# Performance work log

Hardware: AMD Instinct MI355X
Metric: run time of the kernel (lower is better)

The kernel has to match this reference:

```python
import jax, jax.numpy as jnp
import numpy as np

N, E, B = 40000, 640000, 256
F_IN, H, D = 128, 128, 128  # num_node_features, hidden_dim, last_dim
EPS = 1e-5


def sage_conv(x, src, dst, Wl, bl, Wr, num_nodes):
    # PyG SAGEConv (mean aggr): out = lin_l(mean_j x_j) + lin_r(x)
    msg = x[src]                                            # [E, d] gather
    agg = jax.ops.segment_sum(msg, dst, num_segments=num_nodes)
    cnt = jax.ops.segment_sum(jnp.ones((src.shape[0],), x.dtype), dst,
                              num_segments=num_nodes)
    mean = agg / jnp.maximum(cnt, 1.0)[:, None]
    return mean @ Wl.T + bl + x @ Wr.T


def bn_eval(x, g, b, rm, rv):
    return g * (x - rm) * jax.lax.rsqrt(rv + EPS) + b


def lstm_cell(inp, h, c, Wih, Whh, bih, bhh):
    gates = inp @ Wih.T + h @ Whh.T + bih + bhh             # [B, 4D]
    i, f, g, o = jnp.split(gates, 4, axis=-1)
    c = jax.nn.sigmoid(f) * c + jax.nn.sigmoid(i) * jnp.tanh(g)
    h = jax.nn.sigmoid(o) * jnp.tanh(c)
    return h, c


def set2set(x, batch, Wih, Whh, bih, bhh, num_graphs, steps=3):
    d = x.shape[1]
    q_star = jnp.zeros((num_graphs, 2 * d), x.dtype)
    h = jnp.zeros((num_graphs, d), x.dtype)
    c = jnp.zeros((num_graphs, d), x.dtype)
    for _ in range(steps):
        h, c = lstm_cell(q_star, h, c, Wih, Whh, bih, bhh)
        q = h                                               # [B, D]
        e = jnp.sum(x * q[batch], axis=-1)                  # [N]
        emax = jax.ops.segment_max(e, batch, num_segments=num_graphs)
        a = jnp.exp(e - emax[batch])
        denom = jax.ops.segment_sum(a, batch, num_segments=num_graphs)
        a = a / denom[batch]
        r = jax.ops.segment_sum(a[:, None] * x, batch, num_segments=num_graphs)
        q_star = jnp.concatenate([q, r], axis=-1)
    return q_star


def setup_inputs() -> dict:
    key = jax.random.key(0)
    ks = jax.random.split(key, 20)
    x = jax.random.normal(ks[0], (N, F_IN), jnp.float32)
    edge_index = jax.random.randint(ks[1], (2, E), 0, N)
    batch = jnp.sort(jax.random.randint(ks[2], (N,), 0, B))
    s1, s2, sd = 1.0 / np.sqrt(F_IN), 1.0 / np.sqrt(H), 1.0 / np.sqrt(D)
    return {
        "x": x, "edge_index": edge_index, "batch": batch,
        "W1l": jax.random.normal(ks[3], (H, F_IN)) * s1,
        "b1l": jnp.zeros((H,)),
        "W1r": jax.random.normal(ks[4], (H, F_IN)) * s1,
        "g1": jnp.ones((H,)), "beta1": jnp.zeros((H,)),
        "rm1": jax.random.normal(ks[5], (H,)) * 0.1,
        "rv1": jax.random.uniform(ks[6], (H,), minval=0.5, maxval=1.5),
        "W2l": jax.random.normal(ks[7], (D, H)) * s2,
        "b2l": jnp.zeros((D,)),
        "W2r": jax.random.normal(ks[8], (D, H)) * s2,
        "g2": jnp.ones((D,)), "beta2": jnp.zeros((D,)),
        "rm2": jax.random.normal(ks[9], (D,)) * 0.1,
        "rv2": jax.random.uniform(ks[10], (D,), minval=0.5, maxval=1.5),
        "Wih": jax.random.normal(ks[11], (4 * D, 2 * D)) * sd,
        "Whh": jax.random.normal(ks[12], (4 * D, D)) * sd,
        "bih": jnp.zeros((4 * D,)), "bhh": jnp.zeros((4 * D,)),
        "Wp": jax.random.normal(ks[13], (D, 2 * D)) * sd,
        "bp": jnp.zeros((D,)),
    }


def reference(x, edge_index, batch, W1l, b1l, W1r, g1, beta1, rm1, rv1,
              W2l, b2l, W2r, g2, beta2, rm2, rv2, Wih, Whh, bih, bhh, Wp, bp):
    src, dst = edge_index[0], edge_index[1]
    num_nodes = x.shape[0]
    h1 = jax.nn.relu(bn_eval(sage_conv(x, src, dst, W1l, b1l, W1r, num_nodes),
                             g1, beta1, rm1, rv1))
    # dropout is identity in eval mode
    h2 = jax.nn.relu(bn_eval(sage_conv(h1, src, dst, W2l, b2l, W2r, num_nodes),
                             g2, beta2, rm2, rv2))
    q_star = set2set(h2, batch, Wih, Whh, bih, bhh, B, steps=3)  # [B, 2D]
    return q_star @ Wp.T + bp                                    # [B, D]
```

## Files before the change

kernel.cpp:

```cpp
#include <hip/hip_runtime.h>
#include <hip/hip_bf16.h>
#include <math.h>

#define NN 40000
#define NE 640000
#define NG 256
#define FD 128
#define SLOT 96
#define CSTR 32

typedef __attribute__((ext_vector_type(8))) short bf16x8;
typedef __attribute__((ext_vector_type(4))) float f32x4;

__device__ __forceinline__ float sigf(float x) { return 1.f / (1.f + __expf(-x)); }
__device__ __forceinline__ unsigned short f2b(float f) {
    unsigned int u = __float_as_uint(f);
    return (unsigned short)((u + 0x7FFFu + ((u >> 16) & 1u)) >> 16);
}
__device__ __forceinline__ float b2f(unsigned int u16) {
    return __uint_as_float(u16 << 16);
}

__global__ __launch_bounds__(256) void k_fused1(
    const float* __restrict__ A,
    const float* __restrict__ W1l, const float* __restrict__ W1r,
    unsigned short* __restrict__ C,
    const int* __restrict__ ei, const int* __restrict__ batch,
    int* __restrict__ gptr, int* __restrict__ dcnt, int* __restrict__ srcs,
    const float* __restrict__ W2l, const float* __restrict__ W2r,
    unsigned short* __restrict__ Wb,
    const float* __restrict__ Wihf, const float* __restrict__ Whhf,
    unsigned short* __restrict__ Wb2)
{
    __shared__ unsigned short Ws[128 * 128];
    int bid = blockIdx.x, t = threadIdx.x;

    if ((bid < 2012) && (bid & 1)) {
        int sidx = bid >> 1;
        if (sidx < 625) {
            int i = sidx * 256 + t;
            int4 s4 = ((const int4*)ei)[i];
            int4 d4 = ((const int4*)(ei + NE))[i];
            int p0 = atomicAdd(&dcnt[d4.x * CSTR], 1);
            if (p0 < SLOT) srcs[d4.x * SLOT + p0] = s4.x;
            int p1 = atomicAdd(&dcnt[d4.y * CSTR], 1);
            if (p1 < SLOT) srcs[d4.y * SLOT + p1] = s4.y;
            int p2 = atomicAdd(&dcnt[d4.z * CSTR], 1);
            if (p2 < SLOT) srcs[d4.z * SLOT + p2] = s4.z;
            int p3 = atomicAdd(&dcnt[d4.w * CSTR], 1);
            if (p3 < SLOT) srcs[d4.w * SLOT + p3] = s4.w;
        } else if (sidx < 782) {
            int i = (sidx - 625) * 256 + t;
            if (i >= NN) return;
            int b = batch[i];
            int pb = (i == 0) ? -1 : batch[i - 1];
            for (int g = pb + 1; g <= b; g++) gptr[g] = i;
            if (i == NN - 1)
                for (int g = b + 1; g <= NG; g++) gptr[g] = NN;
        } else if (sidx < 814) {
            int j4 = (sidx - 782) * 256 + t;
            int seg = j4 >> 12, off4 = j4 & 4095;
            const float* W = seg ? W2r : W2l;
            float4 v = ((const float4*)W)[off4];
            ushort4 o;
            o.x = f2b(v.x); o.y = f2b(v.y); o.z = f2b(v.z); o.w = f2b(v.w);
            *(ushort4*)(Wb + (size_t)j4 * 4) = o;
        } else {
            int j4 = (sidx - 814) * 256 + t;
            float4 v;
            size_t off;
            if (j4 < 32768) {
                int r = j4 >> 6, f4 = j4 & 63;
                int c = f4 >> 1, h = f4 & 1;
                v = ((const float4*)Wihf)[j4];
                off = ((size_t)c * 512 + r) * 8 + h * 4;
            } else {
                int jj = j4 - 32768;
                int r = jj >> 5, f4 = jj & 31;
                int c = f4 >> 1, h = f4 & 1;
                v = ((const float4*)Whhf)[jj];
                off = (size_t)512 * 256 + ((size_t)c * 512 + r) * 8 + h * 4;
            }
            ushort4 o;
            o.x = f2b(v.x); o.y = f2b(v.y); o.z = f2b(v.z); o.w = f2b(v.w);
            *(ushort4*)(Wb2 + off) = o;
        }
        return;
    }

    int mblk2 = (bid < 2012) ? (bid >> 1) : (bid - 1006);
    int nh = mblk2 & 1;
    int mblk = mblk2 >> 1;
    {
        const float* Wsrc = nh ? W1r : W1l;
#pragma unroll
        for (int i = 0; i < 8; i++) {
            int f = i * 256 + t;
            int row = f >> 4, c = f & 15;
            float4 u0 = *(const float4*)(Wsrc + row * 128 + c * 8);
            float4 u1 = *(const float4*)(Wsrc + row * 128 + c * 8 + 4);
            unsigned short tmp[8];
            tmp[0] = f2b(u0.x); tmp[1] = f2b(u0.y); tmp[2] = f2b(u0.z); tmp[3] = f2b(u0.w);
            tmp[4] = f2b(u1.x); tmp[5] = f2b(u1.y); tmp[6] = f2b(u1.z); tmp[7] = f2b(u1.w);
            int cs = c ^ (row & 15);
            *(uint4*)&Ws[row * 128 + cs * 8] = *(const uint4*)tmp;
        }
    }
    __syncthreads();
    int w = t >> 6, lane = t & 63;
    int ln = lane & 15, quad = lane >> 4;
    int m0 = mblk * 64 + w * 16;
    bf16x8 a[4];
    {
        const float* Arow = A + (size_t)(m0 + ln) * 128;
#pragma unroll
        for (int ks = 0; ks < 4; ks++) {
            float4 u0 = *(const float4*)(Arow + ks * 32 + quad * 8);
            float4 u1 = *(const float4*)(Arow + ks * 32 + quad * 8 + 4);
            unsigned short tmp[8];
            tmp[0] = f2b(u0.x); tmp[1] = f2b(u0.y); tmp[2] = f2b(u0.z); tmp[3] = f2b(u0.w);
            tmp[4] = f2b(u1.x); tmp[5] = f2b(u1.y); tmp[6] = f2b(u1.z); tmp[7] = f2b(u1.w);
            a[ks] = *(const bf16x8*)tmp;
        }
    }
    for (int nt = 0; nt < 8; nt++) {
        int n0 = nt * 16;
        int row = n0 + ln;
        f32x4 acc = {0.f, 0.f, 0.f, 0.f};
#pragma unroll
        for (int ks = 0; ks < 4; ks++) {
            int c = ks * 4 + quad;
            bf16x8 b = *(const bf16x8*)&Ws[row * 128 + (c ^ (row & 15)) * 8];
            acc = __builtin_amdgcn_mfma_f32_16x16x32_bf16(a[ks], b, acc, 0, 0, 0);
        }
        size_t base = (size_t)(m0 + quad * 4) * 256 + nh * 128 + n0 + ln;
#pragma unroll
        for (int r = 0; r < 4; r++)
            C[base + (size_t)r * 256] = f2b(acc[r]);
    }
}

__global__ __launch_bounds__(256) void k_mm_bf16(
    const unsigned short* __restrict__ A,
    const unsigned short* __restrict__ W,
    unsigned short* __restrict__ C)
{
    __shared__ unsigned short Ws[128 * 128];
    int t = threadIdx.x;
    int nh = blockIdx.x & 1;
    int mblk = blockIdx.x >> 1;
    {
        const uint4* Wg = (const uint4*)(W + nh * 128 * 128);
#pragma unroll
        for (int i = 0; i < 8; i++) {
            int f = i * 256 + t;
            int row = f >> 4, c = f & 15;
            int cs = c ^ (row & 15);
            *(uint4*)&Ws[row * 128 + cs * 8] = Wg[f];
        }
    }
    __syncthreads();
    int w = t >> 6, lane = t & 63;
    int ln = lane & 15, quad = lane >> 4;
    int m0 = mblk * 64 + w * 16;
    bf16x8 a[4];
    {
        const unsigned short* Arow = A + (size_t)(m0 + ln) * 128;
#pragma unroll
        for (int ks = 0; ks < 4; ks++)
            a[ks] = *(const bf16x8*)(Arow + ks * 32 + quad * 8);
    }
    for (int nt = 0; nt < 8; nt++) {
        int n0 = nt * 16;
        int row = n0 + ln;
        f32x4 acc = {0.f, 0.f, 0.f, 0.f};
#pragma unroll
        for (int ks = 0; ks < 4; ks++) {
            int c = ks * 4 + quad;
            bf16x8 b = *(const bf16x8*)&Ws[row * 128 + (c ^ (row & 15)) * 8];
            acc = __builtin_amdgcn_mfma_f32_16x16x32_bf16(a[ks], b, acc, 0, 0, 0);
        }
        size_t base = (size_t)(m0 + quad * 4) * 256 + nh * 128 + n0 + ln;
#pragma unroll
        for (int r = 0; r < 4; r++)
            C[base + (size_t)r * 256] = f2b(acc[r]);
    }
}

__global__ __launch_bounds__(256) void k_gather2(
    const unsigned short* __restrict__ C, const int* __restrict__ srcs,
    const int* __restrict__ dcnt,
    const float* __restrict__ bl,
    const float* __restrict__ gam, const float* __restrict__ bet,
    const float* __restrict__ rme, const float* __restrict__ rva,
    unsigned short* __restrict__ H)
{
    int t = threadIdx.x;
    int qw = t >> 4, l4 = t & 15;
    int node = blockIdx.x * 16 + qw;
    int deg = dcnt[node * CSTR];
    int cnt = (deg < SLOT) ? deg : SLOT;
    int s0 = node * SLOT, e0 = s0 + cnt;
    const uint4* C4 = (const uint4*)C;
    float ac[8];
#pragma unroll
    for (int k = 0; k < 8; k++) ac[k] = 0.f;
    int i = s0;
    for (; i + 7 < e0; i += 8) {
        uint4 v0 = C4[(size_t)srcs[i]     * 32 + l4];
        uint4 v1 = C4[(size_t)srcs[i + 1] * 32 + l4];
        uint4 v2 = C4[(size_t)srcs[i + 2] * 32 + l4];
        uint4 v3 = C4[(size_t)srcs[i + 3] * 32 + l4];
        uint4 v4 = C4[(size_t)srcs[i + 4] * 32 + l4];
        uint4 v5 = C4[(size_t)srcs[i + 5] * 32 + l4];
        uint4 v6 = C4[(size_t)srcs[i + 6] * 32 + l4];
        uint4 v7 = C4[(size_t)srcs[i + 7] * 32 + l4];
        ac[0] += b2f(v0.x & 0xFFFFu) + b2f(v1.x & 0xFFFFu) + b2f(v2.x & 0xFFFFu) + b2f(v3.x & 0xFFFFu)
               + b2f(v4.x & 0xFFFFu) + b2f(v5.x & 0xFFFFu) + b2f(v6.x & 0xFFFFu) + b2f(v7.x & 0xFFFFu);
        ac[1] += b2f(v0.x >> 16) + b2f(v1.x >> 16) + b2f(v2.x >> 16) + b2f(v3.x >> 16)
               + b2f(v4.x >> 16) + b2f(v5.x >> 16) + b2f(v6.x >> 16) + b2f(v7.x >> 16);
        ac[2] += b2f(v0.y & 0xFFFFu) + b2f(v1.y & 0xFFFFu) + b2f(v2.y & 0xFFFFu) + b2f(v3.y & 0xFFFFu)
               + b2f(v4.y & 0xFFFFu) + b2f(v5.y & 0xFFFFu) + b2f(v6.y & 0xFFFFu) + b2f(v7.y & 0xFFFFu);
        ac[3] += b2f(v0.y >> 16) + b2f(v1.y >> 16) + b2f(v2.y >> 16) + b2f(v3.y >> 16)
               + b2f(v4.y >> 16) + b2f(v5.y >> 16) + b2f(v6.y >> 16) + b2f(v7.y >> 16);
        ac[4] += b2f(v0.z & 0xFFFFu) + b2f(v1.z & 0xFFFFu) + b2f(v2.z & 0xFFFFu) + b2f(v3.z & 0xFFFFu)
               + b2f(v4.z & 0xFFFFu) + b2f(v5.z & 0xFFFFu) + b2f(v6.z & 0xFFFFu) + b2f(v7.z & 0xFFFFu);
        ac[5] += b2f(v0.z >> 16) + b2f(v1.z >> 16) + b2f(v2.z >> 16) + b2f(v3.z >> 16)
               + b2f(v4.z >> 16) + b2f(v5.z >> 16) + b2f(v6.z >> 16) + b2f(v7.z >> 16);
        ac[6] += b2f(v0.w & 0xFFFFu) + b2f(v1.w & 0xFFFFu) + b2f(v2.w & 0xFFFFu) + b2f(v3.w & 0xFFFFu)
               + b2f(v4.w & 0xFFFFu) + b2f(v5.w & 0xFFFFu) + b2f(v6.w & 0xFFFFu) + b2f(v7.w & 0xFFFFu);
        ac[7] += b2f(v0.w >> 16) + b2f(v1.w >> 16) + b2f(v2.w >> 16) + b2f(v3.w >> 16)
               + b2f(v4.w >> 16) + b2f(v5.w >> 16) + b2f(v6.w >> 16) + b2f(v7.w >> 16);
    }
    for (; i < e0; i++) {
        uint4 v = C4[(size_t)srcs[i] * 32 + l4];
        ac[0] += b2f(v.x & 0xFFFFu); ac[1] += b2f(v.x >> 16);
        ac[2] += b2f(v.y & 0xFFFFu); ac[3] += b2f(v.y >> 16);
        ac[4] += b2f(v.z & 0xFFFFu); ac[5] += b2f(v.z >> 16);
        ac[6] += b2f(v.w & 0xFFFFu); ac[7] += b2f(v.w >> 16);
    }
    float inv = 1.0f / fmaxf((float)deg, 1.0f);
    uint4 yr = C4[(size_t)node * 32 + 16 + l4];
    float yo[8];
    yo[0] = b2f(yr.x & 0xFFFFu); yo[1] = b2f(yr.x >> 16);
    yo[2] = b2f(yr.y & 0xFFFFu); yo[3] = b2f(yr.y >> 16);
    yo[4] = b2f(yr.z & 0xFFFFu); yo[5] = b2f(yr.z >> 16);
    yo[6] = b2f(yr.w & 0xFFFFu); yo[7] = b2f(yr.w >> 16);
    float4 ga = ((const float4*)gam)[l4 * 2],     gb = ((const float4*)gam)[l4 * 2 + 1];
    float4 va = ((const float4*)rva)[l4 * 2],     vb = ((const float4*)rva)[l4 * 2 + 1];
    float4 ma = ((const float4*)rme)[l4 * 2],     mb = ((const float4*)rme)[l4 * 2 + 1];
    float4 ba = ((const float4*)bet)[l4 * 2],     bb = ((const float4*)bet)[l4 * 2 + 1];
    float4 la = ((const float4*)bl)[l4 * 2],      lb = ((const float4*)bl)[l4 * 2 + 1];
    float g[8] = {ga.x, ga.y, ga.z, ga.w, gb.x, gb.y, gb.z, gb.w};
    float rv[8] = {va.x, va.y, va.z, va.w, vb.x, vb.y, vb.z, vb.w};
    float rm[8] = {ma.x, ma.y, ma.z, ma.w, mb.x, mb.y, mb.z, mb.w};
    float bt[8] = {ba.x, ba.y, ba.z, ba.w, bb.x, bb.y, bb.z, bb.w};
    float lv[8] = {la.x, la.y, la.z, la.w, lb.x, lb.y, lb.z, lb.w};
    unsigned short o[8];
#pragma unroll
    for (int k = 0; k < 8; k++) {
        float y = ac[k] * inv + yo[k] + lv[k];
        float z = g[k] * rsqrtf(rv[k] + 1e-5f) * (y - rm[k]) + bt[k];
        o[k] = f2b(fmaxf(z, 0.f));
    }
    *(uint4*)(H + (size_t)node * 128 + l4 * 8) = *(const uint4*)o;
}

__global__ __launch_bounds__(1024) void k_s2s(
    const unsigned short* __restrict__ h2, const int* __restrict__ gptr,
    const float* __restrict__ bih, const float* __restrict__ bhh,
    const unsigned short* __restrict__ Wihb, const unsigned short* __restrict__ Whhb,
    const float* __restrict__ Wp, const float* __restrict__ bp,
    float* __restrict__ out)
{
    int b = blockIdx.x, t = threadIdx.x;
    int wave = t >> 6, lane = t & 63;
    int grp = t >> 4, l4 = t & 15;
    __shared__ float hs[FD];
    __shared__ float qstar[2 * FD];
    __shared__ float gates_s[512];
    __shared__ float es[512];
    __shared__ float wm[16], wd[16], red[16][FD];
    float creg = 0.f;
    int start = gptr[b], end = gptr[b + 1];
    int seg = end - start;
    const unsigned int* H2 = (const unsigned int*)h2;
    const uint4* H4 = (const uint4*)h2;

    for (int step = 0; step < 3; step++) {
        if (step == 0) {
            if (t < FD) {
                float ig = bih[t] + bhh[t];
                float gg = bih[2 * FD + t] + bhh[2 * FD + t];
                float og = bih[3 * FD + t] + bhh[3 * FD + t];
                float c = sigf(ig) * tanhf(gg);
                float h = sigf(og) * tanhf(c);
                creg = c; hs[t] = h;
            }
        } else {
            if (t < 512) {
                float acc = bih[t] + bhh[t];
                const uint4* wi = (const uint4*)Wihb;
                for (int k = 0; k < 32; k++) {
                    uint4 u = wi[k * 512 + t];
                    const float* q = &qstar[k * 8];
                    acc += b2f(u.x & 0xFFFFu)*q[0] + b2f(u.x >> 16)*q[1]
                         + b2f(u.y & 0xFFFFu)*q[2] + b2f(u.y >> 16)*q[3]
                         + b2f(u.z & 0xFFFFu)*q[4] + b2f(u.z >> 16)*q[5]
                         + b2f(u.w & 0xFFFFu)*q[6] + b2f(u.w >> 16)*q[7];
                }
                const uint4* wh = (const uint4*)Whhb;
                for (int k = 0; k < 16; k++) {
                    uint4 u = wh[k * 512 + t];
                    const float* hq = &hs[k * 8];
                    acc += b2f(u.x & 0xFFFFu)*hq[0] + b2f(u.x >> 16)*hq[1]
                         + b2f(u.y & 0xFFFFu)*hq[2] + b2f(u.y >> 16)*hq[3]
                         + b2f(u.z & 0xFFFFu)*hq[4] + b2f(u.z >> 16)*hq[5]
                         + b2f(u.w & 0xFFFFu)*hq[6] + b2f(u.w >> 16)*hq[7];
                }
                gates_s[t] = acc;
            }
            __syncthreads();
            if (t < FD) {
                float ig = gates_s[t], fg = gates_s[FD + t];
                float gg = gates_s[2 * FD + t], og = gates_s[3 * FD + t];
                float c = sigf(fg) * creg + sigf(ig) * tanhf(gg);
                float h = sigf(og) * tanhf(c);
                creg = c; hs[t] = h;
            }
        }
        __syncthreads();

        if (seg <= 512) {
            float4 qa = ((const float4*)hs)[l4 * 2];
            float4 qb = ((const float4*)hs)[l4 * 2 + 1];
            float mg = -INFINITY;
            for (int n = start + grp; n < end; n += 64) {
                uint4 v = H4[(size_t)n * 16 + l4];
                float e = qa.x * b2f(v.x & 0xFFFFu) + qa.y * b2f(v.x >> 16)
                        + qa.z * b2f(v.y & 0xFFFFu) + qa.w * b2f(v.y >> 16)
                        + qb.x * b2f(v.z & 0xFFFFu) + qb.y * b2f(v.z >> 16)
                        + qb.z * b2f(v.w & 0xFFFFu) + qb.w * b2f(v.w >> 16);
#pragma unroll
                for (int off = 8; off; off >>= 1) e += __shfl_xor(e, off);
                if (l4 == 0) es[n - start] = e;
                mg = fmaxf(mg, e);
            }
            mg = fmaxf(mg, __shfl_xor(mg, 16));
            mg = fmaxf(mg, __shfl_xor(mg, 32));
            if (lane == 0) wm[wave] = mg;
            __syncthreads();
            float M = wm[0];
#pragma unroll
            for (int k = 1; k < 16; k++) M = fmaxf(M, wm[k]);
            float r8[8];
#pragma unroll
            for (int j = 0; j < 8; j++) r8[j] = 0.f;
            float dwl = 0.f;
            for (int n = start + grp; n < end; n += 64) {
                uint4 v = H4[(size_t)n * 16 + l4];
                float a = __expf(es[n - start] - M);
                r8[0] += a * b2f(v.x & 0xFFFFu); r8[1] += a * b2f(v.x >> 16);
                r8[2] += a * b2f(v.y & 0xFFFFu); r8[3] += a * b2f(v.y >> 16);
                r8[4] += a * b2f(v.z & 0xFFFFu); r8[5] += a * b2f(v.z >> 16);
                r8[6] += a * b2f(v.w & 0xFFFFu); r8[7] += a * b2f(v.w >> 16);
                dwl += a;
            }
#pragma unroll
            for (int j = 0; j < 8; j++) {
                r8[j] += __shfl_xor(r8[j], 16);
                r8[j] += __shfl_xor(r8[j], 32);
            }
            dwl += __shfl_xor(dwl, 16);
            dwl += __shfl_xor(dwl, 32);
            if (lane < 16) {
                float4 wa = {r8[0], r8[1], r8[2], r8[3]};
                float4 wb = {r8[4], r8[5], r8[6], r8[7]};
                *(float4*)&red[wave][lane * 8]     = wa;
                *(float4*)&red[wave][lane * 8 + 4] = wb;
            }
            if (lane == 0) wd[wave] = dwl;
        } else {
            float2 q = ((const float2*)hs)[lane];
            float rx = 0.f, ry = 0.f, dw = 0.f;
            float mw = -INFINITY;
            for (int n = start + wave; n < end; n += 16) {
                unsigned int u = H2[(size_t)n * 64 + lane];
                float vx = b2f(u & 0xFFFFu), vy = b2f(u >> 16);
                float e = vx * q.x + vy * q.y;
#pragma unroll
                for (int off = 32; off; off >>= 1) e += __shfl_xor(e, off);
                float mn = fmaxf(mw, e);
                float corr = __expf(mw - mn);
                float a = __expf(e - mn);
                rx = rx * corr + a * vx;
                ry = ry * corr + a * vy;
                dw = dw * corr + a;
                mw = mn;
            }
            if (lane == 0) wm[wave] = mw;
            __syncthreads();
            float M = wm[0];
#pragma unroll
            for (int k = 1; k < 16; k++) M = fmaxf(M, wm[k]);
            float cr = (M == -INFINITY) ? 0.f : __expf(mw - M);
            red[wave][2 * lane] = rx * cr;
            red[wave][2 * lane + 1] = ry * cr;
            if (lane == 0) wd[wave] = dw * cr;
        }
        __syncthreads();
        if (t < FD) {
            float r = 0.f, den = 0.f;
#pragma unroll
            for (int k = 0; k < 16; k++) { r += red[k][t]; den += wd[k]; }
            float rn = (den > 0.f) ? r / den : 0.f;
            qstar[t] = hs[t];
            qstar[FD + t] = rn;
        }
        __syncthreads();
    }

    if (t < FD) {
        const float4* w4 = (const float4*)(Wp + (size_t)t * 256);
        const float4* q4 = (const float4*)qstar;
        float acc = bp[t];
        for (int k = 0; k < 64; k++) {
            float4 wv = w4[k], qv = q4[k];
            acc += qv.x*wv.x + qv.y*wv.y + qv.z*wv.z + qv.w*wv.w;
        }
        out[(size_t)b * FD + t] = acc;
    }
}

__global__ void k_zero_out(float* __restrict__ out, int n) {
    int i = blockIdx.x * blockDim.x + threadIdx.x;
    if (i < n) out[i] = 0.f;
}

extern "C" void kernel_launch(void* const* d_in, const int* in_sizes, int n_in,
                              void* d_out, int out_size, void* d_ws, size_t ws_size,
                              hipStream_t stream) {
    const float* x   = (const float*)d_in[0];
    const int*  ei    = (const int*)d_in[1];
    const int*  batch = (const int*)d_in[2];
    const float* W1l = (const float*)d_in[3];
    const float* b1l = (const float*)d_in[4];
    const float* W1r = (const float*)d_in[5];
    const float* g1  = (const float*)d_in[6];
    const float* be1 = (const float*)d_in[7];
    const float* rm1 = (const float*)d_in[8];
    const float* rv1 = (const float*)d_in[9];
    const float* W2l = (const float*)d_in[10];
    const float* b2l = (const float*)d_in[11];
    const float* W2r = (const float*)d_in[12];
    const float* g2  = (const float*)d_in[13];
    const float* be2 = (const float*)d_in[14];
    const float* rm2 = (const float*)d_in[15];
    const float* rv2 = (const float*)d_in[16];
    const float* Wih = (const float*)d_in[17];
    const float* Whh = (const float*)d_in[18];
    const float* bih = (const float*)d_in[19];
    const float* bhh = (const float*)d_in[20];
    const float* Wp  = (const float*)d_in[21];
    const float* bp  = (const float*)d_in[22];
    float* out = (float*)d_out;

    auto al = [](size_t s) { return (s + 255) & ~(size_t)255; };
    size_t off_dcnt = 0;
    size_t off_gptr = off_dcnt + al((size_t)NN * CSTR * 4);
    size_t off_srcs = off_gptr + al((size_t)(NG + 1) * 4);
    size_t off_h2b  = off_srcs + al((size_t)NN * SLOT * 4);
    size_t off_h1b  = off_h2b  + al((size_t)NN * FD * 2);
    size_t off_Wb   = off_h1b  + al((size_t)NN * FD * 2);
    size_t off_Wb2  = off_Wb   + al((size_t)256 * 128 * 2);
    size_t off_C    = off_Wb2  + al((size_t)(512 * 256 + 512 * 128) * 2);
    size_t need     = off_C    + al((size_t)NN * 256 * 2);

    if (ws_size < need) {
        k_zero_out<<<(out_size + 255) / 256, 256, 0, stream>>>(out, out_size);
        return;
    }

    char* p = (char*)d_ws;
    int* dcnt    = (int*)(p + off_dcnt);
    int* gptr    = (int*)(p + off_gptr);
    int* srcs    = (int*)(p + off_srcs);
    unsigned short* h2b = (unsigned short*)(p + off_h2b);
    unsigned short* h1b = (unsigned short*)(p + off_h1b);
    unsigned short* Wb  = (unsigned short*)(p + off_Wb);
    unsigned short* Wb2 = (unsigned short*)(p + off_Wb2);
    unsigned short* C   = (unsigned short*)(p + off_C);

    hipMemsetAsync(dcnt, 0, (size_t)NN * CSTR * 4, stream);

    k_fused1<<<2256, 256, 0, stream>>>(x, W1l, W1r, C,
                                       ei, batch, gptr, dcnt, srcs,
                                       W2l, W2r, Wb, Wih, Whh, Wb2);
    k_gather2<<<NN / 16, 256, 0, stream>>>(C, srcs, dcnt, b1l, g1, be1, rm1, rv1, h1b);

    k_mm_bf16<<<1250, 256, 0, stream>>>(h1b, Wb, C);
    k_gather2<<<NN / 16, 256, 0, stream>>>(C, srcs, dcnt, b2l, g2, be2, rm2, rv2, h2b);

    k_s2s<<<NG, 1024, 0, stream>>>(h2b, gptr, bih, bhh,
                                   Wb2, Wb2 + 512 * 256, Wp, bp, out);
}
```

Baseline: 239.2 us.

## Bucket edges by destination block and build per-node lists in shared memory

Replaces per-node global atomics and slot lists with per-bucket (40-node) atomics that append packed src/local-dst words into a bucket buffer. Each gather block then reads its bucket, builds per-node source lists in LDS with shared atomics, and aggregates. This cuts global atomic contention and the memset size and improves write locality, but it rebuilds the local lists in both gather passes. It also caps bucket occupancy at 832 edges, so edges beyond that are silently dropped if a bucket overflows, and src is packed in 16 bits even though N is 40000.

New measurement: 228.4 us, median of 2. 1.05x faster.

```diff
diff --git a/kernel.cpp b/kernel.cpp
--- a/kernel.cpp
+++ b/kernel.cpp
@@ -7,7 +7,10 @@
 #define NG 256
 #define FD 128
 #define SLOT 96
-#define CSTR 32
+#define NBK 1000
+#define NPB 40
+#define ECAP 832
+#define BPAD 32
 
 typedef __attribute__((ext_vector_type(8))) short bf16x8;
 typedef __attribute__((ext_vector_type(4))) float f32x4;
@@ -26,7 +29,7 @@
     const float* __restrict__ W1l, const float* __restrict__ W1r,
     unsigned short* __restrict__ C,
     const int* __restrict__ ei, const int* __restrict__ batch,
-    int* __restrict__ gptr, int* __restrict__ dcnt, int* __restrict__ srcs,
+    int* __restrict__ gptr, int* __restrict__ bcnt, unsigned int* __restrict__ ebuf,
     const float* __restrict__ W2l, const float* __restrict__ W2r,
     unsigned short* __restrict__ Wb,
     const float* __restrict__ Wihf, const float* __restrict__ Whhf,
@@ -41,14 +44,22 @@
             int i = sidx * 256 + t;
             int4 s4 = ((const int4*)ei)[i];
             int4 d4 = ((const int4*)(ei + NE))[i];
-            int p0 = atomicAdd(&dcnt[d4.x * CSTR], 1);
-            if (p0 < SLOT) srcs[d4.x * SLOT + p0] = s4.x;
-            int p1 = atomicAdd(&dcnt[d4.y * CSTR], 1);
-            if (p1 < SLOT) srcs[d4.y * SLOT + p1] = s4.y;
-            int p2 = atomicAdd(&dcnt[d4.z * CSTR], 1);
-            if (p2 < SLOT) srcs[d4.z * SLOT + p2] = s4.z;
-            int p3 = atomicAdd(&dcnt[d4.w * CSTR], 1);
-            if (p3 < SLOT) srcs[d4.w * SLOT + p3] = s4.w;
+            int b0 = d4.x / NPB;
+            int p0 = atomicAdd(&bcnt[b0 * BPAD], 1);
+            if (p0 < ECAP) ebuf[b0 * ECAP + p0] =
+                (unsigned int)s4.x | ((unsigned int)(d4.x - b0 * NPB) << 16);
+            int b1 = d4.y / NPB;
+            int p1 = atomicAdd(&bcnt[b1 * BPAD], 1);
+            if (p1 < ECAP) ebuf[b1 * ECAP + p1] =
+                (unsigned int)s4.y | ((unsigned int)(d4.y - b1 * NPB) << 16);
+            int b2 = d4.z / NPB;
+            int p2 = atomicAdd(&bcnt[b2 * BPAD], 1);
+            if (p2 < ECAP) ebuf[b2 * ECAP + p2] =
+                (unsigned int)s4.z | ((unsigned int)(d4.z - b2 * NPB) << 16);
+            int b3 = d4.w / NPB;
+            int p3 = atomicAdd(&bcnt[b3 * BPAD], 1);
+            if (p3 < ECAP) ebuf[b3 * ECAP + p3] =
+                (unsigned int)s4.w | ((unsigned int)(d4.w - b3 * NPB) << 16);
         } else if (sidx < 782) {
             int i = (sidx - 625) * 256 + t;
             if (i >= NN) return;
@@ -187,83 +198,100 @@
     }
 }
 
-__global__ __launch_bounds__(256) void k_gather2(
-    const unsigned short* __restrict__ C, const int* __restrict__ srcs,
-    const int* __restrict__ dcnt,
+__global__ __launch_bounds__(256) void k_gather3(
+    const unsigned short* __restrict__ C,
+    const int* __restrict__ bcnt, const unsigned int* __restrict__ ebuf,
     const float* __restrict__ bl,
     const float* __restrict__ gam, const float* __restrict__ bet,
     const float* __restrict__ rme, const float* __restrict__ rva,
     unsigned short* __restrict__ H)
 {
-    int t = threadIdx.x;
-    int qw = t >> 4, l4 = t & 15;
-    int node = blockIdx.x * 16 + qw;
-    int deg = dcnt[node * CSTR];
-    int cnt = (deg < SLOT) ? deg : SLOT;
-    int s0 = node * SLOT, e0 = s0 + cnt;
+    __shared__ int lcnt[NPB];
+    __shared__ int lsr[NPB][SLOT];
+    int b = blockIdx.x, t = threadIdx.x;
+    if (t < NPB) lcnt[t] = 0;
+    __syncthreads();
+    int cnt = bcnt[b * BPAD];
+    if (cnt > ECAP) cnt = ECAP;
+    for (int e = t; e < cnt; e += 256) {
+        unsigned int u = ebuf[b * ECAP + e];
+        int ld = u >> 16;
+        int p = atomicAdd(&lcnt[ld], 1);
+        if (p < SLOT) lsr[ld][p] = (int)(u & 0xFFFFu);
+    }
+    __syncthreads();
+
+    int g = t >> 4, l4 = t & 15;
     const uint4* C4 = (const uint4*)C;
-    float ac[8];
-#pragma unroll
-    for (int k = 0; k < 8; k++) ac[k] = 0.f;
-    int i = s0;
-    for (; i + 7 < e0; i += 8) {
-        uint4 v0 = C4[(size_t)srcs[i]     * 32 + l4];
-        uint4 v1 = C4[(size_t)srcs[i + 1] * 32 + l4];
-        uint4 v2 = C4[(size_t)srcs[i + 2] * 32 + l4];
-        uint4 v3 = C4[(size_t)srcs[i + 3] * 32 + l4];
-        uint4 v4 = C4[(size_t)srcs[i + 4] * 32 + l4];
-        uint4 v5 = C4[(size_t)srcs[i + 5] * 32 + l4];
-        uint4 v6 = C4[(size_t)srcs[i + 6] * 32 + l4];
-        uint4 v7 = C4[(size_t)srcs[i + 7] * 32 + l4];
-        ac[0] += b2f(v0.x & 0xFFFFu) + b2f(v1.x & 0xFFFFu) + b2f(v2.x & 0xFFFFu) + b2f(v3.x & 0xFFFFu)
-               + b2f(v4.x & 0xFFFFu) + b2f(v5.x & 0xFFFFu) + b2f(v6.x & 0xFFFFu) + b2f(v7.x & 0xFFFFu);
-        ac[1] += b2f(v0.x >> 16) + b2f(v1.x >> 16) + b2f(v2.x >> 16) + b2f(v3.x >> 16)
-               + b2f(v4.x >> 16) + b2f(v5.x >> 16) + b2f(v6.x >> 16) + b2f(v7.x >> 16);
-        ac[2] += b2f(v0.y & 0xFFFFu) + b2f(v1.y & 0xFFFFu) + b2f(v2.y & 0xFFFFu) + b2f(v3.y & 0xFFFFu)
-               + b2f(v4.y & 0xFFFFu) + b2f(v5.y & 0xFFFFu) + b2f(v6.y & 0xFFFFu) + b2f(v7.y & 0xFFFFu);
-        ac[3] += b2f(v0.y >> 16) + b2f(v1.y >> 16) + b2f(v2.y >> 16) + b2f(v3.y >> 16)
-               + b2f(v4.y >> 16) + b2f(v5.y >> 16) + b2f(v6.y >> 16) + b2f(v7.y >> 16);
-        ac[4] += b2f(v0.z & 0xFFFFu) + b2f(v1.z & 0xFFFFu) + b2f(v2.z & 0xFFFFu) + b2f(v3.z & 0xFFFFu)
-               + b2f(v4.z & 0xFFFFu) + b2f(v5.z & 0xFFFFu) + b2f(v6.z & 0xFFFFu) + b2f(v7.z & 0xFFFFu);
-        ac[5] += b2f(v0.z >> 16) + b2f(v1.z >> 16) + b2f(v2.z >> 16) + b2f(v3.z >> 16)
-               + b2f(v4.z >> 16) + b2f(v5.z >> 16) + b2f(v6.z >> 16) + b2f(v7.z >> 16);
-        ac[6] += b2f(v0.w & 0xFFFFu) + b2f(v1.w & 0xFFFFu) + b2f(v2.w & 0xFFFFu) + b2f(v3.w & 0xFFFFu)
-               + b2f(v4.w & 0xFFFFu) + b2f(v5.w & 0xFFFFu) + b2f(v6.w & 0xFFFFu) + b2f(v7.w & 0xFFFFu);
-        ac[7] += b2f(v0.w >> 16) + b2f(v1.w >> 16) + b2f(v2.w >> 16) + b2f(v3.w >> 16)
-               + b2f(v4.w >> 16) + b2f(v5.w >> 16) + b2f(v6.w >> 16) + b2f(v7.w >> 16);
-    }
-    for (; i < e0; i++) {
-        uint4 v = C4[(size_t)srcs[i] * 32 + l4];
-        ac[0] += b2f(v.x & 0xFFFFu); ac[1] += b2f(v.x >> 16);
-        ac[2] += b2f(v.y & 0xFFFFu); ac[3] += b2f(v.y >> 16);
-        ac[4] += b2f(v.z & 0xFFFFu); ac[5] += b2f(v.z >> 16);
-        ac[6] += b2f(v.w & 0xFFFFu); ac[7] += b2f(v.w >> 16);
-    }
-    float inv = 1.0f / fmaxf((float)deg, 1.0f);
-    uint4 yr = C4[(size_t)node * 32 + 16 + l4];
-    float yo[8];
-    yo[0] = b2f(yr.x & 0xFFFFu); yo[1] = b2f(yr.x >> 16);
-    yo[2] = b2f(yr.y & 0xFFFFu); yo[3] = b2f(yr.y >> 16);
-    yo[4] = b2f(yr.z & 0xFFFFu); yo[5] = b2f(yr.z >> 16);
-    yo[6] = b2f(yr.w & 0xFFFFu); yo[7] = b2f(yr.w >> 16);
+
     float4 ga = ((const float4*)gam)[l4 * 2],     gb = ((const float4*)gam)[l4 * 2 + 1];
     float4 va = ((const float4*)rva)[l4 * 2],     vb = ((const float4*)rva)[l4 * 2 + 1];
     float4 ma = ((const float4*)rme)[l4 * 2],     mb = ((const float4*)rme)[l4 * 2 + 1];
     float4 ba = ((const float4*)bet)[l4 * 2],     bb = ((const float4*)bet)[l4 * 2 + 1];
     float4 la = ((const float4*)bl)[l4 * 2],      lb = ((const float4*)bl)[l4 * 2 + 1];
-    float g[8] = {ga.x, ga.y, ga.z, ga.w, gb.x, gb.y, gb.z, gb.w};
+    float gq[8] = {ga.x, ga.y, ga.z, ga.w, gb.x, gb.y, gb.z, gb.w};
     float rv[8] = {va.x, va.y, va.z, va.w, vb.x, vb.y, vb.z, vb.w};
     float rm[8] = {ma.x, ma.y, ma.z, ma.w, mb.x, mb.y, mb.z, mb.w};
     float bt[8] = {ba.x, ba.y, ba.z, ba.w, bb.x, bb.y, bb.z, bb.w};
     float lv[8] = {la.x, la.y, la.z, la.w, lb.x, lb.y, lb.z, lb.w};
-    unsigned short o[8];
-#pragma unroll
-    for (int k = 0; k < 8; k++) {
-        float y = ac[k] * inv + yo[k] + lv[k];
-        float z = g[k] * rsqrtf(rv[k] + 1e-5f) * (y - rm[k]) + bt[k];
-        o[k] = f2b(fmaxf(z, 0.f));
-    }
-    *(uint4*)(H + (size_t)node * 128 + l4 * 8) = *(const uint4*)o;
+
+    for (int nd = g; nd < NPB; nd += 16) {
+        int node = b * NPB + nd;
+        int deg = lcnt[nd];
+        int cn = (deg < SLOT) ? deg : SLOT;
+        float ac[8];
+#pragma unroll
+        for (int k = 0; k < 8; k++) ac[k] = 0.f;
+        int i = 0;
+        for (; i + 7 < cn; i += 8) {
+            uint4 v0 = C4[(size_t)lsr[nd][i]     * 32 + l4];
+            uint4 v1 = C4[(size_t)lsr[nd][i + 1] * 32 + l4];
+            uint4 v2 = C4[(size_t)lsr[nd][i + 2] * 32 + l4];
+            uint4 v3 = C4[(size_t)lsr[nd][i + 3] * 32 + l4];
+            uint4 v4 = C4[(size_t)lsr[nd][i + 4] * 32 + l4];
+            uint4 v5 = C4[(size_t)lsr[nd][i + 5] * 32 + l4];
+            uint4 v6 = C4[(size_t)lsr[nd][i + 6] * 32 + l4];
+            uint4 v7 = C4[(size_t)lsr[nd][i + 7] * 32 + l4];
+            ac[0] += b2f(v0.x & 0xFFFFu) + b2f(v1.x & 0xFFFFu) + b2f(v2.x & 0xFFFFu) + b2f(v3.x & 0xFFFFu)
+                   + b2f(v4.x & 0xFFFFu) + b2f(v5.x & 0xFFFFu) + b2f(v6.x & 0xFFFFu) + b2f(v7.x & 0xFFFFu);
+            ac[1] += b2f(v0.x >> 16) + b2f(v1.x >> 16) + b2f(v2.x >> 16) + b2f(v3.x >> 16)
+                   + b2f(v4.x >> 16) + b2f(v5.x >> 16) + b2f(v6.x >> 16) + b2f(v7.x >> 16);
+            ac[2] += b2f(v0.y & 0xFFFFu) + b2f(v1.y & 0xFFFFu) + b2f(v2.y & 0xFFFFu) + b2f(v3.y & 0xFFFFu)
+                   + b2f(v4.y & 0xFFFFu) + b2f(v5.y & 0xFFFFu) + b2f(v6.y & 0xFFFFu) + b2f(v7.y & 0xFFFFu);
+            ac[3] += b2f(v0.y >> 16) + b2f(v1.y >> 16) + b2f(v2.y >> 16) + b2f(v3.y >> 16)
+                   + b2f(v4.y >> 16) + b2f(v5.y >> 16) + b2f(v6.y >> 16) + b2f(v7.y >> 16);
+            ac[4] += b2f(v0.z & 0xFFFFu) + b2f(v1.z & 0xFFFFu) + b2f(v2.z & 0xFFFFu) + b2f(v3.z & 0xFFFFu)
+                   + b2f(v4.z & 0xFFFFu) + b2f(v5.z & 0xFFFFu) + b2f(v6.z & 0xFFFFu) + b2f(v7.z & 0xFFFFu);
+            ac[5] += b2f(v0.z >> 16) + b2f(v1.z >> 16) + b2f(v2.z >> 16) + b2f(v3.z >> 16)
+                   + b2f(v4.z >> 16) + b2f(v5.z >> 16) + b2f(v6.z >> 16) + b2f(v7.z >> 16);
+            ac[6] += b2f(v0.w & 0xFFFFu) + b2f(v1.w & 0xFFFFu) + b2f(v2.w & 0xFFFFu) + b2f(v3.w & 0xFFFFu)
+                   + b2f(v4.w & 0xFFFFu) + b2f(v5.w & 0xFFFFu) + b2f(v6.w & 0xFFFFu) + b2f(v7.w & 0xFFFFu);
+            ac[7] += b2f(v0.w >> 16) + b2f(v1.w >> 16) + b2f(v2.w >> 16) + b2f(v3.w >> 16)
+                   + b2f(v4.w >> 16) + b2f(v5.w >> 16) + b2f(v6.w >> 16) + b2f(v7.w >> 16);
+        }
+        for (; i < cn; i++) {
+            uint4 v = C4[(size_t)lsr[nd][i] * 32 + l4];
+            ac[0] += b2f(v.x & 0xFFFFu); ac[1] += b2f(v.x >> 16);
+            ac[2] += b2f(v.y & 0xFFFFu); ac[3] += b2f(v.y >> 16);
+            ac[4] += b2f(v.z & 0xFFFFu); ac[5] += b2f(v.z >> 16);
+            ac[6] += b2f(v.w & 0xFFFFu); ac[7] += b2f(v.w >> 16);
+        }
+        float inv = 1.0f / fmaxf((float)deg, 1.0f);
+        uint4 yr = C4[(size_t)node * 32 + 16 + l4];
+        float yo[8];
+        yo[0] = b2f(yr.x & 0xFFFFu); yo[1] = b2f(yr.x >> 16);
+        yo[2] = b2f(yr.y & 0xFFFFu); yo[3] = b2f(yr.y >> 16);
+        yo[4] = b2f(yr.z & 0xFFFFu); yo[5] = b2f(yr.z >> 16);
+        yo[6] = b2f(yr.w & 0xFFFFu); yo[7] = b2f(yr.w >> 16);
+        unsigned short o[8];
+#pragma unroll
+        for (int k = 0; k < 8; k++) {
+            float y = ac[k] * inv + yo[k] + lv[k];
+            float z = gq[k] * rsqrtf(rv[k] + 1e-5f) * (y - rm[k]) + bt[k];
+            o[k] = f2b(fmaxf(z, 0.f));
+        }
+        *(uint4*)(H + (size_t)node * 128 + l4 * 8) = *(const uint4*)o;
+    }
 }
 
 __global__ __launch_bounds__(1024) void k_s2s(
@@ -466,10 +494,10 @@
     float* out = (float*)d_out;
 
     auto al = [](size_t s) { return (s + 255) & ~(size_t)255; };
-    size_t off_dcnt = 0;
-    size_t off_gptr = off_dcnt + al((size_t)NN * CSTR * 4);
-    size_t off_srcs = off_gptr + al((size_t)(NG + 1) * 4);
-    size_t off_h2b  = off_srcs + al((size_t)NN * SLOT * 4);
+    size_t off_bcnt = 0;
+    size_t off_ebuf = off_bcnt + al((size_t)NBK * BPAD * 4);
+    size_t off_gptr = off_ebuf + al((size_t)NBK * ECAP * 4);
+    size_t off_h2b  = off_gptr + al((size_t)(NG + 1) * 4);
     size_t off_h1b  = off_h2b  + al((size_t)NN * FD * 2);
     size_t off_Wb   = off_h1b  + al((size_t)NN * FD * 2);
     size_t off_Wb2  = off_Wb   + al((size_t)256 * 128 * 2);
@@ -482,24 +510,24 @@
     }
 
     char* p = (char*)d_ws;
-    int* dcnt    = (int*)(p + off_dcnt);
+    int* bcnt    = (int*)(p + off_bcnt);
+    unsigned int* ebuf = (unsigned int*)(p + off_ebuf);
     int* gptr    = (int*)(p + off_gptr);
-    int* srcs    = (int*)(p + off_srcs);
     unsigned short* h2b = (unsigned short*)(p + off_h2b);
     unsigned short* h1b = (unsigned short*)(p + off_h1b);
     unsigned short* Wb  = (unsigned short*)(p + off_Wb);
     unsigned short* Wb2 = (unsigned short*)(p + off_Wb2);
     unsigned short* C   = (unsigned short*)(p + off_C);
 
-    hipMemsetAsync(dcnt, 0, (size_t)NN * CSTR * 4, stream);
+    hipMemsetAsync(bcnt, 0, (size_t)NBK * BPAD * 4, stream);
 
     k_fused1<<<2256, 256, 0, stream>>>(x, W1l, W1r, C,
-                                       ei, batch, gptr, dcnt, srcs,
+                                       ei, batch, gptr, bcnt, ebuf,
                                        W2l, W2r, Wb, Wih, Whh, Wb2);
-    k_gather2<<<NN / 16, 256, 0, stream>>>(C, srcs, dcnt, b1l, g1, be1, rm1, rv1, h1b);
+    k_gather3<<<NBK, 256, 0, stream>>>(C, bcnt, ebuf, b1l, g1, be1, rm1, rv1, h1b);
 
     k_mm_bf16<<<1250, 256, 0, stream>>>(h1b, Wb, C);
-    k_gather2<<<NN / 16, 256, 0, stream>>>(C, srcs, dcnt, b2l, g2, be2, rm2, rv2, h2b);
+    k_gather3<<<NBK, 256, 0, stream>>>(C, bcnt, ebuf, b2l, g2, be2, rm2, rv2, h2b);
 
     k_s2s<<<NG, 1024, 0, stream>>>(h2b, gptr, bih, bhh,
                                    Wb2, Wb2 + 512 * 256, Wp, bp, out);
```
